# Kernel tuning notes

Hardware: AMD Instinct MI355X
Metric: run time of the kernel (lower is better)

Reference implementation:

```python
import jax, jax.numpy as jnp
import numpy as np

D_MODEL = 1024
D_FF = 4096
N_EXPERTS = 8
B, S = 4, 2048


def setup_inputs() -> dict:
    key = jax.random.key(0)
    ks = jax.random.split(key, 6)
    x = jax.random.normal(ks[0], (B, S, D_MODEL), dtype=jnp.float32)
    # router: nn.Linear(d_model, num_experts) with bias (default torch init ~ small)
    gate_W = jax.random.normal(ks[1], (N_EXPERTS, D_MODEL), dtype=jnp.float32) * 0.02
    gate_b = jnp.zeros((N_EXPERTS,), dtype=jnp.float32)
    # SwiGLU expert weights, bias-free; torch Linear stores [out, in]
    Wg = jax.random.normal(ks[2], (N_EXPERTS, D_FF, D_MODEL), dtype=jnp.float32) * 0.02
    W1 = jax.random.normal(ks[3], (N_EXPERTS, D_FF, D_MODEL), dtype=jnp.float32) * 0.02
    W2 = jax.random.normal(ks[4], (N_EXPERTS, D_MODEL, D_FF), dtype=jnp.float32) * (0.02 / np.sqrt(2.0))
    return {"x": x, "gate_W": gate_W, "gate_b": gate_b, "Wg": Wg, "W1": W1, "W2": W2,
            "num_experts_per_token": 2}


def reference(x, gate_W, gate_b, Wg, W1, W2, num_experts_per_token):
    """Eval-mode ExpertFeedForward: top-k gating + per-expert SwiGLU + weighted combine."""
    Bb, Ss, D = x.shape
    E = gate_W.shape[0]
    T = Bb * Ss
    xt = x.reshape(T, D)  # [T, D] tokens

    # router logits and top-k softmax over selected experts
    logits = xt @ gate_W.T + gate_b              # [T, E]
    scores, idx = jax.lax.top_k(logits, num_experts_per_token)  # [T, k]
    probs = jax.nn.softmax(scores, axis=-1)      # softmax over top-k only

    # combine weights per (token, expert): scatter top-k probs into dense [T, E]
    tok = jnp.arange(T)[:, None]
    cw = jnp.zeros((T, E), dtype=x.dtype).at[tok, idx].add(probs)  # [T, E]

    out = jnp.zeros_like(xt)
    for e in range(E):  # small fixed expert count
        gate = jax.nn.silu(xt @ Wg[e].T)         # [T, d_ff]
        val = xt @ W1[e].T                       # [T, d_ff]
        y = (gate * val) @ W2[e].T               # [T, D]
        out = out + y * cw[:, e:e + 1]
    return out.reshape(Bb, Ss, D)
```

## Files before the change

### kernel.cpp

```cpp
#include <hip/hip_runtime.h>

#define T_TOKENS 8192
#define D_MODEL  1024
#define D_FF     4096
#define N_EXP    8

#define BM 128
#define BN 128
#define BK 32

typedef __attribute__((ext_vector_type(8))) short bf16x8;
typedef __attribute__((ext_vector_type(4))) float f32x4;

__device__ __forceinline__ unsigned short f2bf(float f) {
    unsigned int u = __float_as_uint(f);
    u += 0x7fffu + ((u >> 16) & 1u);
    return (unsigned short)(u >> 16);
}

__device__ __forceinline__ void gld16(const unsigned short* g, unsigned short* l) {
    __builtin_amdgcn_global_load_lds(
        (const __attribute__((address_space(1))) unsigned int*)g,
        (__attribute__((address_space(3))) unsigned int*)l, 16, 0, 0);
}

__global__ void cvt_kernel(const float* __restrict__ src, unsigned short* __restrict__ dst) {
    size_t i = ((size_t)blockIdx.x * 256 + threadIdx.x) * 8;
    float4 a = *(const float4*)(src + i);
    float4 b = *(const float4*)(src + i + 4);
    union { unsigned short u[8]; uint4 v; } r;
    r.u[0] = f2bf(a.x); r.u[1] = f2bf(a.y); r.u[2] = f2bf(a.z); r.u[3] = f2bf(a.w);
    r.u[4] = f2bf(b.x); r.u[5] = f2bf(b.y); r.u[6] = f2bf(b.z); r.u[7] = f2bf(b.w);
    *(uint4*)(dst + i) = r.v;
}

__global__ void router_kernel(const float* __restrict__ x, const float* __restrict__ gW,
                              const float* __restrict__ gb, int* __restrict__ counts,
                              int* __restrict__ top_e, float* __restrict__ top_p) {
    int t    = blockIdx.x * 4 + (threadIdx.x >> 6);
    int lane = threadIdx.x & 63;
    const float* xr = x + (size_t)t * D_MODEL;
    float acc[N_EXP];
#pragma unroll
    for (int e = 0; e < N_EXP; e++) acc[e] = 0.f;
    for (int i = 0; i < D_MODEL / 64; i++) {
        float xv = xr[lane + i * 64];
#pragma unroll
        for (int e = 0; e < N_EXP; e++) acc[e] += xv * gW[e * D_MODEL + lane + i * 64];
    }
#pragma unroll
    for (int e = 0; e < N_EXP; e++) {
#pragma unroll
        for (int off = 32; off > 0; off >>= 1) acc[e] += __shfl_down(acc[e], off, 64);
    }
    if (lane == 0) {
#pragma unroll
        for (int e = 0; e < N_EXP; e++) acc[e] += gb[e];
        int e0 = 0;
#pragma unroll
        for (int e = 1; e < N_EXP; e++) if (acc[e] > acc[e0]) e0 = e;
        int e1 = (e0 == 0) ? 1 : 0;
#pragma unroll
        for (int e = 0; e < N_EXP; e++) if (e != e0 && e != e1 && acc[e] > acc[e1]) e1 = e;
        float z1 = __expf(acc[e1] - acc[e0]);
        float s  = 1.f + z1;
        top_e[t * 2]     = e0;
        top_e[t * 2 + 1] = e1;
        top_p[t * 2]     = 1.f / s;
        top_p[t * 2 + 1] = z1 / s;
        atomicAdd(&counts[e0], 1);
        atomicAdd(&counts[e1], 1);
    }
}

__global__ void prefix_kernel(const int* __restrict__ counts, int* __restrict__ offsets,
                              int* __restrict__ cursor) {
    if (threadIdx.x == 0) {
        int s = 0;
        for (int e = 0; e < N_EXP; e++) { offsets[e] = s; cursor[e] = s; s += counts[e]; }
    }
}

__global__ void scatter_kernel(const int* __restrict__ top_e, const float* __restrict__ top_p,
                               int* __restrict__ cursor, int* __restrict__ row_map,
                               float* __restrict__ row_prob) {
    int t = blockIdx.x * 256 + threadIdx.x;
#pragma unroll
    for (int j = 0; j < 2; j++) {
        int e  = top_e[t * 2 + j];
        int pos = atomicAdd(&cursor[e], 1);
        row_map[pos]  = t;
        row_prob[pos] = top_p[t * 2 + j];
    }
}

__global__ void gather_x_kernel(const float* __restrict__ x, const int* __restrict__ row_map,
                                unsigned short* __restrict__ xg) {
    int pos = blockIdx.x * 2 + (threadIdx.x >> 7);
    int c   = (threadIdx.x & 127) * 8;
    int t   = row_map[pos];
    float4 a = *(const float4*)(x + (size_t)t * D_MODEL + c);
    float4 b = *(const float4*)(x + (size_t)t * D_MODEL + c + 4);
    union { unsigned short u[8]; uint4 v; } r;
    r.u[0] = f2bf(a.x); r.u[1] = f2bf(a.y); r.u[2] = f2bf(a.z); r.u[3] = f2bf(a.w);
    r.u[4] = f2bf(b.x); r.u[5] = f2bf(b.y); r.u[6] = f2bf(b.z); r.u[7] = f2bf(b.w);
    *(uint4*)(xg + (size_t)pos * D_MODEL + c) = r.v;
}


__launch_bounds__(256, 2)
__global__ void gemm1_kernel(const unsigned short* __restrict__ xg,
                             const unsigned short* __restrict__ wgb,
                             const unsigned short* __restrict__ w1b,
                             const int* __restrict__ counts, const int* __restrict__ offsets,
                             const float* __restrict__ row_prob,
                             unsigned short* __restrict__ hbuf) {
    int e   = blockIdx.z;
    int cnt = counts[e];
    int m0  = blockIdx.y * BM;
    if (m0 >= cnt) return;
    int base = offsets[e];
    int n0   = blockIdx.x * BN;
    int tid  = threadIdx.x;
    int wave = tid >> 6, lane = tid & 63;

    __shared__ unsigned short As[BM * BK];
    __shared__ unsigned short Bg[BN * BK];
    __shared__ unsigned short Bv[BN * BK];
    __shared__ float prb[BM];

    if (tid < BM) {
        int i = m0 + tid; if (i > cnt - 1) i = cnt - 1;
        prb[tid] = row_prob[base + i];
    }

    const unsigned short* wg = wgb + (size_t)e * D_FF * D_MODEL;
    const unsigned short* w1 = w1b + (size_t)e * D_FF * D_MODEL;

    const unsigned short* gA[2]; const unsigned short* gG[2]; const unsigned short* gV[2];
    unsigned short* lA[2]; unsigned short* lG[2]; unsigned short* lV[2];
#pragma unroll
    for (int l = 0; l < 2; l++) {
        int cell = wave * 64 + l * 256 + lane;
        int row  = cell >> 2;
        int kb   = (cell & 3) ^ (row & 3);
        int ra = m0 + row; if (ra > cnt - 1) ra = cnt - 1;
        gA[l] = xg + (size_t)(base + ra) * D_MODEL + kb * 8;
        gG[l] = wg + (size_t)(n0 + row) * D_MODEL + kb * 8;
        gV[l] = w1 + (size_t)(n0 + row) * D_MODEL + kb * 8;
        int c0 = wave * 64 + l * 256;
        lA[l] = As + c0 * 8;
        lG[l] = Bg + c0 * 8;
        lV[l] = Bv + c0 * 8;
    }

    int wm = (wave >> 1) * 64, wn = (wave & 1) * 64;
    int lm = lane & 15, lq = lane >> 4;
    int swz = lq ^ (lm & 3);
    const bf16x8* aP = (const bf16x8*)(As + ((wm + lm) * 4 + swz) * 8);
    const bf16x8* gP = (const bf16x8*)(Bg + ((wn + lm) * 4 + swz) * 8);
    const bf16x8* vP = (const bf16x8*)(Bv + ((wn + lm) * 4 + swz) * 8);

    f32x4 accG[4][4], accV[4][4];
#pragma unroll
    for (int i = 0; i < 4; i++)
#pragma unroll
        for (int j = 0; j < 4; j++) { accG[i][j] = (f32x4)0.f; accV[i][j] = (f32x4)0.f; }

    for (int kk = 0; kk < D_MODEL; kk += BK) {
        gld16(gA[0], lA[0]); gld16(gA[1], lA[1]);
        gld16(gG[0], lG[0]); gld16(gG[1], lG[1]);
        gld16(gV[0], lV[0]); gld16(gV[1], lV[1]);
        gA[0] += BK; gA[1] += BK; gG[0] += BK; gG[1] += BK; gV[0] += BK; gV[1] += BK;
        __syncthreads();

        bf16x8 aF[4], bgF[4], bvF[4];
#pragma unroll
        for (int mi = 0; mi < 4; mi++) aF[mi] = aP[mi * 64];
#pragma unroll
        for (int ni = 0; ni < 4; ni++) { bgF[ni] = gP[ni * 64]; bvF[ni] = vP[ni * 64]; }
#pragma unroll
        for (int mi = 0; mi < 4; mi++)
#pragma unroll
            for (int ni = 0; ni < 4; ni++) {
                accG[mi][ni] = __builtin_amdgcn_mfma_f32_16x16x32_bf16(aF[mi], bgF[ni], accG[mi][ni], 0, 0, 0);
                accV[mi][ni] = __builtin_amdgcn_mfma_f32_16x16x32_bf16(aF[mi], bvF[ni], accV[mi][ni], 0, 0, 0);
            }
        __syncthreads();
    }

    size_t hrow_base = (size_t)(base + m0);
#pragma unroll
    for (int mi = 0; mi < 4; mi++) {
#pragma unroll
        for (int r = 0; r < 4; r++) {
            int mrow = wm + mi * 16 + lq * 4 + r;
            if (m0 + mrow < cnt) {
                float p = prb[mrow];
                unsigned short* hp = hbuf + (hrow_base + mrow) * D_FF + n0 + wn;
#pragma unroll
                for (int ni = 0; ni < 4; ni++) {
                    float g = accG[mi][ni][r], v = accV[mi][ni][r];
                    float sg = g / (1.f + __expf(-g));
                    hp[ni * 16 + lm] = f2bf(sg * v * p);
                }
            }
        }
    }
}

__launch_bounds__(256, 2)
__global__ void gemm2_kernel(const unsigned short* __restrict__ hbuf,
                             const unsigned short* __restrict__ w2b,
                             const int* __restrict__ counts, const int* __restrict__ offsets,
                             const int* __restrict__ row_map,
                             float* __restrict__ out) {
    int e   = blockIdx.z;
    int cnt = counts[e];
    int m0  = blockIdx.y * BM;
    if (m0 >= cnt) return;
    int base = offsets[e];
    int n0   = blockIdx.x * BN;
    int tid  = threadIdx.x;
    int wave = tid >> 6, lane = tid & 63;

    __shared__ unsigned short As[BM * BK];
    __shared__ unsigned short Bs[BN * BK];
    __shared__ int tok[BM];

    if (tid < BM) {
        int i = m0 + tid; if (i > cnt - 1) i = cnt - 1;
        tok[tid] = row_map[base + i];
    }

    const unsigned short* w2 = w2b + (size_t)e * D_MODEL * D_FF;

    const unsigned short* gA[2]; const unsigned short* gB[2];
    unsigned short* lA[2]; unsigned short* lB[2];
#pragma unroll
    for (int l = 0; l < 2; l++) {
        int cell = wave * 64 + l * 256 + lane;
        int row  = cell >> 2;
        int kb   = (cell & 3) ^ (row & 3);
        int ra = m0 + row; if (ra > cnt - 1) ra = cnt - 1;
        gA[l] = hbuf + (size_t)(base + ra) * D_FF + kb * 8;
        gB[l] = w2 + (size_t)(n0 + row) * D_FF + kb * 8;
        int c0 = wave * 64 + l * 256;
        lA[l] = As + c0 * 8;
        lB[l] = Bs + c0 * 8;
    }

    int wm = (wave >> 1) * 64, wn = (wave & 1) * 64;
    int lm = lane & 15, lq = lane >> 4;
    int swz = lq ^ (lm & 3);
    const bf16x8* aP = (const bf16x8*)(As + ((wm + lm) * 4 + swz) * 8);
    const bf16x8* bP = (const bf16x8*)(Bs + ((wn + lm) * 4 + swz) * 8);

    f32x4 acc[4][4];
#pragma unroll
    for (int i = 0; i < 4; i++)
#pragma unroll
        for (int j = 0; j < 4; j++) acc[i][j] = (f32x4)0.f;

    for (int kk = 0; kk < D_FF; kk += BK) {
        gld16(gA[0], lA[0]); gld16(gA[1], lA[1]);
        gld16(gB[0], lB[0]); gld16(gB[1], lB[1]);
        gA[0] += BK; gA[1] += BK; gB[0] += BK; gB[1] += BK;
        __syncthreads();

        bf16x8 aF[4], bF[4];
#pragma unroll
        for (int mi = 0; mi < 4; mi++) aF[mi] = aP[mi * 64];
#pragma unroll
        for (int ni = 0; ni < 4; ni++) bF[ni] = bP[ni * 64];
#pragma unroll
        for (int mi = 0; mi < 4; mi++)
#pragma unroll
            for (int ni = 0; ni < 4; ni++)
                acc[mi][ni] = __builtin_amdgcn_mfma_f32_16x16x32_bf16(aF[mi], bF[ni], acc[mi][ni], 0, 0, 0);
        __syncthreads();
    }

#pragma unroll
    for (int mi = 0; mi < 4; mi++) {
#pragma unroll
        for (int r = 0; r < 4; r++) {
            int mrow = wm + mi * 16 + lq * 4 + r;
            if (m0 + mrow < cnt) {
                int t = tok[mrow];
                float* op = out + (size_t)t * D_MODEL + n0 + wn;
#pragma unroll
                for (int ni = 0; ni < 4; ni++)
                    atomicAdd(&op[ni * 16 + lm], acc[mi][ni][r]);
            }
        }
    }
}

extern "C" void kernel_launch(void* const* d_in, const int* in_sizes, int n_in,
                              void* d_out, int out_size, void* d_ws, size_t ws_size,
                              hipStream_t stream) {
    const float* x  = (const float*)d_in[0];
    const float* gW = (const float*)d_in[1];
    const float* gb = (const float*)d_in[2];
    const float* Wg = (const float*)d_in[3];
    const float* W1 = (const float*)d_in[4];
    const float* W2 = (const float*)d_in[5];
    float* out = (float*)d_out;

    char* ws = (char*)d_ws;
    const size_t MiB = 1024 * 1024;
    int*   counts   = (int*)ws;
    int*   offsets  = (int*)(ws + 64);
    int*   cursor   = (int*)(ws + 128);
    int*   row_map  = (int*)(ws + 256);
    float* row_prob = (float*)(ws + 256 + 65536);
    int*   top_e    = (int*)(ws + 256 + 2 * 65536);
    float* top_p    = (float*)(ws + 256 + 3 * 65536);
    unsigned short* wgb  = (unsigned short*)(ws + 1 * MiB);
    unsigned short* w1b  = (unsigned short*)(ws + 65 * MiB);
    unsigned short* xg   = (unsigned short*)(ws + 129 * MiB);
    unsigned short* hbuf = (unsigned short*)(ws + 161 * MiB);
    unsigned short* w2b  = wgb;

    hipMemsetAsync(ws, 0, 256, stream);
    hipMemsetAsync(d_out, 0, (size_t)T_TOKENS * D_MODEL * sizeof(float), stream);

    cvt_kernel<<<16384, 256, 0, stream>>>(Wg, wgb);
    cvt_kernel<<<16384, 256, 0, stream>>>(W1, w1b);
    router_kernel<<<T_TOKENS / 4, 256, 0, stream>>>(x, gW, gb, counts, top_e, top_p);
    prefix_kernel<<<1, 64, 0, stream>>>(counts, offsets, cursor);
    scatter_kernel<<<T_TOKENS / 256, 256, 0, stream>>>(top_e, top_p, cursor, row_map, row_prob);
    gather_x_kernel<<<T_TOKENS, 256, 0, stream>>>(x, row_map, xg);
    gemm1_kernel<<<dim3(D_FF / BN, T_TOKENS / BM, N_EXP), 256, 0, stream>>>(
        xg, wgb, w1b, counts, offsets, row_prob, hbuf);
    cvt_kernel<<<16384, 256, 0, stream>>>(W2, w2b);
    gemm2_kernel<<<dim3(D_MODEL / BN, T_TOKENS / BM, N_EXP), 256, 0, stream>>>(
        hbuf, w2b, counts, offsets, row_map, out);
}
```

Baseline: 1.300 ms.

## Replace atomic scatter-add with bf16 per-row output and separate combine kernel

The second GEMM now writes its per-expert rows as bf16 into a workspace buffer instead of doing float atomicAdd into the output, and a new combine kernel sums each token's two expert rows. This also drops the output memset. It additionally swaps grid x/y so consecutive blocks walk M instead of N, and adds an extra XOR term to the LDS swizzle to reduce bank conflicts. The combine step rounds partial sums to bf16, which costs some accuracy, and it reads the rows back in a scattered pattern.

```diff
diff --git a/kernel.cpp b/kernel.cpp
--- a/kernel.cpp
+++ b/kernel.cpp
@@ -16,6 +16,10 @@
     unsigned int u = __float_as_uint(f);
     u += 0x7fffu + ((u >> 16) & 1u);
     return (unsigned short)(u >> 16);
+}
+__device__ __forceinline__ float bf2f(unsigned short h) {
+    unsigned int u = (unsigned int)h << 16;
+    return __uint_as_float(u);
 }
 
 __device__ __forceinline__ void gld16(const unsigned short* g, unsigned short* l) {
@@ -83,7 +87,7 @@
 
 __global__ void scatter_kernel(const int* __restrict__ top_e, const float* __restrict__ top_p,
                                int* __restrict__ cursor, int* __restrict__ row_map,
-                               float* __restrict__ row_prob) {
+                               float* __restrict__ row_prob, int* __restrict__ pos_of) {
     int t = blockIdx.x * 256 + threadIdx.x;
 #pragma unroll
     for (int j = 0; j < 2; j++) {
@@ -91,6 +95,7 @@
         int pos = atomicAdd(&cursor[e], 1);
         row_map[pos]  = t;
         row_prob[pos] = top_p[t * 2 + j];
+        pos_of[t * 2 + j] = pos;
     }
 }
 
@@ -117,10 +122,10 @@
                              unsigned short* __restrict__ hbuf) {
     int e   = blockIdx.z;
     int cnt = counts[e];
-    int m0  = blockIdx.y * BM;
+    int m0  = blockIdx.x * BM;
     if (m0 >= cnt) return;
     int base = offsets[e];
-    int n0   = blockIdx.x * BN;
+    int n0   = blockIdx.y * BN;
     int tid  = threadIdx.x;
     int wave = tid >> 6, lane = tid & 63;
 
@@ -143,7 +148,7 @@
     for (int l = 0; l < 2; l++) {
         int cell = wave * 64 + l * 256 + lane;
         int row  = cell >> 2;
-        int kb   = (cell & 3) ^ (row & 3);
+        int kb   = (cell & 3) ^ (row & 3) ^ ((row >> 2) & 3);
         int ra = m0 + row; if (ra > cnt - 1) ra = cnt - 1;
         gA[l] = xg + (size_t)(base + ra) * D_MODEL + kb * 8;
         gG[l] = wg + (size_t)(n0 + row) * D_MODEL + kb * 8;
@@ -156,7 +161,7 @@
 
     int wm = (wave >> 1) * 64, wn = (wave & 1) * 64;
     int lm = lane & 15, lq = lane >> 4;
-    int swz = lq ^ (lm & 3);
+    int swz = lq ^ (lm & 3) ^ ((lm >> 2) & 3);
     const bf16x8* aP = (const bf16x8*)(As + ((wm + lm) * 4 + swz) * 8);
     const bf16x8* gP = (const bf16x8*)(Bg + ((wn + lm) * 4 + swz) * 8);
     const bf16x8* vP = (const bf16x8*)(Bv + ((wn + lm) * 4 + swz) * 8);
@@ -213,25 +218,18 @@
 __global__ void gemm2_kernel(const unsigned short* __restrict__ hbuf,
                              const unsigned short* __restrict__ w2b,
                              const int* __restrict__ counts, const int* __restrict__ offsets,
-                             const int* __restrict__ row_map,
-                             float* __restrict__ out) {
+                             unsigned short* __restrict__ ybuf) {
     int e   = blockIdx.z;
     int cnt = counts[e];
-    int m0  = blockIdx.y * BM;
+    int m0  = blockIdx.x * BM;
     if (m0 >= cnt) return;
     int base = offsets[e];
-    int n0   = blockIdx.x * BN;
+    int n0   = blockIdx.y * BN;
     int tid  = threadIdx.x;
     int wave = tid >> 6, lane = tid & 63;
 
     __shared__ unsigned short As[BM * BK];
     __shared__ unsigned short Bs[BN * BK];
-    __shared__ int tok[BM];
-
-    if (tid < BM) {
-        int i = m0 + tid; if (i > cnt - 1) i = cnt - 1;
-        tok[tid] = row_map[base + i];
-    }
 
     const unsigned short* w2 = w2b + (size_t)e * D_MODEL * D_FF;
 
@@ -241,7 +239,7 @@
     for (int l = 0; l < 2; l++) {
         int cell = wave * 64 + l * 256 + lane;
         int row  = cell >> 2;
-        int kb   = (cell & 3) ^ (row & 3);
+        int kb   = (cell & 3) ^ (row & 3) ^ ((row >> 2) & 3);
         int ra = m0 + row; if (ra > cnt - 1) ra = cnt - 1;
         gA[l] = hbuf + (size_t)(base + ra) * D_FF + kb * 8;
         gB[l] = w2 + (size_t)(n0 + row) * D_FF + kb * 8;
@@ -252,7 +250,7 @@
 
     int wm = (wave >> 1) * 64, wn = (wave & 1) * 64;
     int lm = lane & 15, lq = lane >> 4;
-    int swz = lq ^ (lm & 3);
+    int swz = lq ^ (lm & 3) ^ ((lm >> 2) & 3);
     const bf16x8* aP = (const bf16x8*)(As + ((wm + lm) * 4 + swz) * 8);
     const bf16x8* bP = (const bf16x8*)(Bs + ((wn + lm) * 4 + swz) * 8);
 
@@ -287,14 +285,29 @@
         for (int r = 0; r < 4; r++) {
             int mrow = wm + mi * 16 + lq * 4 + r;
             if (m0 + mrow < cnt) {
-                int t = tok[mrow];
-                float* op = out + (size_t)t * D_MODEL + n0 + wn;
+                unsigned short* yp = ybuf + (size_t)(base + m0 + mrow) * D_MODEL + n0 + wn;
 #pragma unroll
                 for (int ni = 0; ni < 4; ni++)
-                    atomicAdd(&op[ni * 16 + lm], acc[mi][ni][r]);
+                    yp[ni * 16 + lm] = f2bf(acc[mi][ni][r]);
             }
         }
     }
+}
+
+__global__ void combine_kernel(const unsigned short* __restrict__ ybuf,
+                               const int* __restrict__ pos_of,
+                               float* __restrict__ out) {
+    int t = blockIdx.x;
+    int c = threadIdx.x * 4;
+    int p0 = pos_of[t * 2], p1 = pos_of[t * 2 + 1];
+    ushort4 a = *(const ushort4*)(ybuf + (size_t)p0 * D_MODEL + c);
+    ushort4 b = *(const ushort4*)(ybuf + (size_t)p1 * D_MODEL + c);
+    float4 o;
+    o.x = bf2f(a.x) + bf2f(b.x);
+    o.y = bf2f(a.y) + bf2f(b.y);
+    o.z = bf2f(a.z) + bf2f(b.z);
+    o.w = bf2f(a.w) + bf2f(b.w);
+    *(float4*)(out + (size_t)t * D_MODEL + c) = o;
 }
 
 extern "C" void kernel_launch(void* const* d_in, const int* in_sizes, int n_in,
@@ -317,24 +330,26 @@
     float* row_prob = (float*)(ws + 256 + 65536);
     int*   top_e    = (int*)(ws + 256 + 2 * 65536);
     float* top_p    = (float*)(ws + 256 + 3 * 65536);
+    int*   pos_of   = (int*)(ws + 256 + 4 * 65536);
     unsigned short* wgb  = (unsigned short*)(ws + 1 * MiB);
     unsigned short* w1b  = (unsigned short*)(ws + 65 * MiB);
     unsigned short* xg   = (unsigned short*)(ws + 129 * MiB);
     unsigned short* hbuf = (unsigned short*)(ws + 161 * MiB);
     unsigned short* w2b  = wgb;
+    unsigned short* ybuf = xg;
 
     hipMemsetAsync(ws, 0, 256, stream);
-    hipMemsetAsync(d_out, 0, (size_t)T_TOKENS * D_MODEL * sizeof(float), stream);
 
     cvt_kernel<<<16384, 256, 0, stream>>>(Wg, wgb);
     cvt_kernel<<<16384, 256, 0, stream>>>(W1, w1b);
     router_kernel<<<T_TOKENS / 4, 256, 0, stream>>>(x, gW, gb, counts, top_e, top_p);
     prefix_kernel<<<1, 64, 0, stream>>>(counts, offsets, cursor);
-    scatter_kernel<<<T_TOKENS / 256, 256, 0, stream>>>(top_e, top_p, cursor, row_map, row_prob);
+    scatter_kernel<<<T_TOKENS / 256, 256, 0, stream>>>(top_e, top_p, cursor, row_map, row_prob, pos_of);
     gather_x_kernel<<<T_TOKENS, 256, 0, stream>>>(x, row_map, xg);
-    gemm1_kernel<<<dim3(D_FF / BN, T_TOKENS / BM, N_EXP), 256, 0, stream>>>(
+    gemm1_kernel<<<dim3(T_TOKENS / BM, D_FF / BN, N_EXP), 256, 0, stream>>>(
         xg, wgb, w1b, counts, offsets, row_prob, hbuf);
     cvt_kernel<<<16384, 256, 0, stream>>>(W2, w2b);
-    gemm2_kernel<<<dim3(D_MODEL / BN, T_TOKENS / BM, N_EXP), 256, 0, stream>>>(
-        hbuf, w2b, counts, offsets, row_map, out);
-}
+    gemm2_kernel<<<dim3(T_TOKENS / BM, D_MODEL / BN, N_EXP), 256, 0, stream>>>(
+        hbuf, w2b, counts, offsets, ybuf);
+    combine_kernel<<<T_TOKENS, 256, 0, stream>>>(ybuf, pos_of, out);
+}
```

Measured after the change: 1.580 ms. 1.22x slower.
